# Kernel tuning notes

Hardware: AMD Instinct MI355X
Metric: run time of the kernel (lower is better)

Reference implementation:

```python
import jax, jax.numpy as jnp
import numpy as np

EPS = 1e-12  # clamp for sqrt stability in Gram-matrix distance

def _pairwise_euclid(X, Y):
    # [B,D],[M,D] -> [B,M] Euclidean distances via Gram trick (avoids [B,M,D] diff tensor)
    x2 = jnp.sum(X * X, axis=-1, keepdims=True)        # [B,1]
    y2 = jnp.sum(Y * Y, axis=-1)[None, :]              # [1,M]
    sq = x2 + y2 - 2.0 * (X @ Y.T)
    return jnp.sqrt(jnp.maximum(sq, EPS))

def setup_inputs() -> dict:
    key = jax.random.key(0)
    k1, k2, k3 = jax.random.split(key, 3)
    B, D = 4096, 128
    return {
        "rep_anchor": jax.random.normal(k1, (B, D), dtype=jnp.float32),
        "rep_pos": jax.random.normal(k2, (B, D), dtype=jnp.float32),
        "rep_neg": jax.random.normal(k3, (B, D), dtype=jnp.float32),
    }

def reference(rep_anchor, rep_pos, rep_neg):
    B = rep_anchor.shape[0]
    # distance_pos[i] = ||a_i - p_i||_2 (elementwise rows, like F.pairwise_distance)
    diff = rep_anchor - rep_pos
    distance_pos = jnp.sqrt(jnp.maximum(jnp.sum(diff * diff, axis=-1), EPS))  # [B]

    big = jnp.asarray(jnp.finfo(rep_anchor.dtype).max, rep_anchor.dtype)
    eye = jnp.eye(B, dtype=bool)
    # anchor-as-negative: exclude self (index i)
    d_aa = jnp.where(eye, big, _pairwise_euclid(rep_anchor, rep_anchor))  # [B,B]
    # pos-as-negative: rep_pos[i] is excluded for anchor i
    d_ap = jnp.where(eye, big, _pairwise_euclid(rep_anchor, rep_pos))    # [B,B]
    # all of rep_neg are negatives
    d_an = _pairwise_euclid(rep_anchor, rep_neg)                          # [B,B]

    hardest_neg = jnp.minimum(jnp.minimum(d_aa.min(axis=1), d_ap.min(axis=1)), d_an.min(axis=1))  # [B]
    # log1p(exp(x)) == softplus, computed stably
    loss_in_batch = jnp.logaddexp(0.0, distance_pos - hardest_neg)
    return jnp.mean(loss_in_batch)
```

## Files before the change

### kernel.cpp

```cpp
#include <hip/hip_runtime.h>
#include <math.h>

#define BDIM 4096
#define DDIM 128
#define EPSF 1e-12f
#define TI 128
#define TJc 128
#define NSPLIT 16
#define NSLICE (NSPLIT * 2)
#define ITILES (BDIM / TI)
#define JT 6
#define FLT_BIG 3.402823466e+38f
#define MATSZ (BDIM * DDIM)
#define YBUF (TJc * DDIM)

typedef __attribute__((ext_vector_type(8))) _Float16 f16x8;
typedef __attribute__((ext_vector_type(16))) float f32x16;

__device__ __forceinline__ void gload_lds16(const void* g, void* l) {
    __builtin_amdgcn_global_load_lds(
        (const __attribute__((address_space(1))) unsigned int*)(uintptr_t)g,
        (__attribute__((address_space(3))) unsigned int*)(unsigned int)(uintptr_t)l,
        16, 0, 0);
}

__device__ __forceinline__ unsigned int pack2h(float x, float y) {
    _Float16 hx = (_Float16)x, hy = (_Float16)y;
    unsigned short ux, uy;
    __builtin_memcpy(&ux, &hx, 2);
    __builtin_memcpy(&uy, &hy, 2);
    return (unsigned int)ux | ((unsigned int)uy << 16);
}

__global__ __launch_bounds__(256) void prep_kernel(
    const float* __restrict__ A, const float* __restrict__ P,
    const float* __restrict__ N, ushort* __restrict__ Xf,
    float* __restrict__ a2, float* __restrict__ p2,
    float* __restrict__ n2, float* __restrict__ dpos) {
    int row = (blockIdx.x * blockDim.x + threadIdx.x) >> 6;
    int lane = threadIdx.x & 63;
    if (row >= BDIM) return;
    const float2 av = *(const float2*)&A[row * DDIM + lane * 2];
    const float2 pv = *(const float2*)&P[row * DDIM + lane * 2];
    const float2 nv = *(const float2*)&N[row * DDIM + lane * 2];
    *(unsigned int*)&Xf[0 * MATSZ + row * DDIM + lane * 2] = pack2h(av.x, av.y);
    *(unsigned int*)&Xf[1 * MATSZ + row * DDIM + lane * 2] = pack2h(pv.x, pv.y);
    *(unsigned int*)&Xf[2 * MATSZ + row * DDIM + lane * 2] = pack2h(nv.x, nv.y);
    float sa = av.x * av.x + av.y * av.y;
    float sp = pv.x * pv.x + pv.y * pv.y;
    float sn = nv.x * nv.x + nv.y * nv.y;
    float dx = av.x - pv.x, dy = av.y - pv.y;
    float sd = dx * dx + dy * dy;
    #pragma unroll
    for (int off = 32; off; off >>= 1) {
        sa += __shfl_down(sa, off);
        sp += __shfl_down(sp, off);
        sn += __shfl_down(sn, off);
        sd += __shfl_down(sd, off);
    }
    if (lane == 0) {
        a2[row] = sa;
        p2[row] = sp;
        n2[row] = sn;
        dpos[row] = sqrtf(fmaxf(sd, EPSF));
    }
}

__global__ __launch_bounds__(256, 2) void minsq_kernel(
    const ushort* __restrict__ Xf,
    const float* __restrict__ a2, const float* __restrict__ p2,
    const float* __restrict__ n2, float* __restrict__ partial) {
    __shared__ __align__(16) ushort Y[2][YBUF];

    const int tid = threadIdx.x;
    const int w = tid >> 6;
    const int lane = tid & 63;
    const int rg = w >> 1;
    const int ch = w & 1;
    const int iTile = blockIdx.x;
    const int split = blockIdx.y;
    const int i0 = iTile * TI;
    const int jt0 = split * JT;
    const int sub = lane >> 4, s = lane & 15;

    {
        int m = jt0 >> 5, tc = jt0 & 31;
        const ushort* g = Xf + (size_t)m * MATSZ + (size_t)tc * TJc * DDIM;
        #pragma unroll
        for (int q = 0; q < 8; ++q) {
            int r = w * 32 + q * 4 + sub;
            int sp = s ^ (r & 15);
            gload_lds16(g + (size_t)r * DDIM + sp * 8,
                        &Y[0][(w * 32 + q * 4) * DDIM]);
        }
    }
    f16x8 a0[8], a1[8];
    {
        const ushort* r0 = Xf + (size_t)(i0 + rg * 64 + (lane & 31)) * DDIM;
        const ushort* r1 = r0 + 32 * DDIM;
        #pragma unroll
        for (int t = 0; t < 8; ++t) {
            int sl = t * 2 + (lane >> 5);
            a0[t] = *(const f16x8*)(r0 + sl * 8);
            a1[t] = *(const f16x8*)(r1 + sl * 8);
        }
    }
    float y2h0[JT], y2h1[JT];
    #pragma unroll
    for (int t = 0; t < JT; ++t) {
        int jt = jt0 + t, m = jt >> 5, tc = jt & 31;
        const float* y2g = (m == 0) ? a2 : ((m == 1) ? p2 : n2);
        int jb = tc * TJc + ch * 64 + (lane & 31);
        y2h0[t] = 0.5f * y2g[jb];
        y2h1[t] = 0.5f * y2g[jb + 32];
    }

    float minv0[16], minv1[16];
    #pragma unroll
    for (int g = 0; g < 16; ++g) { minv0[g] = FLT_BIG; minv1[g] = FLT_BIG; }

    #pragma unroll
    for (int idx = 0; idx < JT; ++idx) {
        if (idx + 1 < JT) {
            int jn = jt0 + idx + 1, m = jn >> 5, tc = jn & 31;
            const ushort* g = Xf + (size_t)m * MATSZ + (size_t)tc * TJc * DDIM;
            #pragma unroll
            for (int q = 0; q < 8; ++q) {
                int r = w * 32 + q * 4 + sub;
                int sp = s ^ (r & 15);
                gload_lds16(g + (size_t)r * DDIM + sp * 8,
                            &Y[(idx + 1) & 1][(w * 32 + q * 4) * DDIM]);
            }
            asm volatile("s_waitcnt vmcnt(8)" ::: "memory");
        } else {
            asm volatile("s_waitcnt vmcnt(0)" ::: "memory");
        }
        __builtin_amdgcn_sched_barrier(0);
        __builtin_amdgcn_s_barrier();
        __builtin_amdgcn_sched_barrier(0);

        const ushort* buf = &Y[idx & 1][0];
        const int rB0 = ch * 64 + (lane & 31);
        const int rB1 = rB0 + 32;
        f32x16 acc00 = {}, acc01 = {}, acc10 = {}, acc11 = {};
        __builtin_amdgcn_s_setprio(1);
        #pragma unroll
        for (int t = 0; t < 8; ++t) {
            int sl = t * 2 + (lane >> 5);
            f16x8 b0 = *(const f16x8*)&buf[rB0 * DDIM + (sl ^ (rB0 & 15)) * 8];
            f16x8 b1 = *(const f16x8*)&buf[rB1 * DDIM + (sl ^ (rB1 & 15)) * 8];
            acc00 = __builtin_amdgcn_mfma_f32_32x32x16_f16(a0[t], b0, acc00, 0, 0, 0);
            acc10 = __builtin_amdgcn_mfma_f32_32x32x16_f16(a1[t], b0, acc10, 0, 0, 0);
            acc01 = __builtin_amdgcn_mfma_f32_32x32x16_f16(a0[t], b1, acc01, 0, 0, 0);
            acc11 = __builtin_amdgcn_mfma_f32_32x32x16_f16(a1[t], b1, acc11, 0, 0, 0);
        }
        __builtin_amdgcn_s_setprio(0);

        {
            int jt = jt0 + idx, m = jt >> 5, tc = jt & 31;
            float yh0 = y2h0[idx], yh1 = y2h1[idx];
            if (m < 2 && tc == iTile) {
                int jg0 = tc * TJc + ch * 64 + (lane & 31);
                int jg1 = jg0 + 32;
                #pragma unroll
                for (int g = 0; g < 16; ++g) {
                    int rloc = (g & 3) + 8 * (g >> 2) + 4 * (lane >> 5);
                    int ig0 = i0 + rg * 64 + rloc;
                    int ig1 = ig0 + 32;
                    float c;
                    c = yh0 - acc00[g]; if (ig0 == jg0) c = FLT_BIG;
                    minv0[g] = fminf(minv0[g], c);
                    c = yh1 - acc01[g]; if (ig0 == jg1) c = FLT_BIG;
                    minv0[g] = fminf(minv0[g], c);
                    c = yh0 - acc10[g]; if (ig1 == jg0) c = FLT_BIG;
                    minv1[g] = fminf(minv1[g], c);
                    c = yh1 - acc11[g]; if (ig1 == jg1) c = FLT_BIG;
                    minv1[g] = fminf(minv1[g], c);
                }
            } else {
                #pragma unroll
                for (int g = 0; g < 16; ++g) {
                    minv0[g] = fminf(minv0[g], fminf(yh0 - acc00[g], yh1 - acc01[g]));
                    minv1[g] = fminf(minv1[g], fminf(yh0 - acc10[g], yh1 - acc11[g]));
                }
            }
        }
        __builtin_amdgcn_s_barrier();
    }

    #pragma unroll
    for (int off = 1; off < 32; off <<= 1) {
        #pragma unroll
        for (int g = 0; g < 16; ++g) {
            minv0[g] = fminf(minv0[g], __shfl_xor(minv0[g], off));
            minv1[g] = fminf(minv1[g], __shfl_xor(minv1[g], off));
        }
    }
    if ((lane & 31) == 0) {
        int hi = lane >> 5;
        int slice = split * 2 + ch;
        #pragma unroll
        for (int g = 0; g < 16; ++g) {
            int rloc = (g & 3) + 8 * (g >> 2) + 4 * hi;
            int ig = i0 + rg * 64 + rloc;
            partial[(size_t)ig * NSLICE + slice] = minv0[g];
            partial[(size_t)(ig + 32) * NSLICE + slice] = minv1[g];
        }
    }
}

__global__ __launch_bounds__(256) void lossA_kernel(
    const float* __restrict__ partial, const float* __restrict__ a2,
    const float* __restrict__ dpos, float* __restrict__ bsum) {
    __shared__ float red[4];
    int i = blockIdx.x * 256 + threadIdx.x;
    const float4* pr = (const float4*)&partial[(size_t)i * NSLICE];
    float mv = FLT_BIG;
    #pragma unroll
    for (int q = 0; q < NSLICE / 4; ++q) {
        float4 v = pr[q];
        mv = fminf(mv, fminf(fminf(v.x, v.y), fminf(v.z, v.w)));
    }
    float h2 = a2[i] + 2.0f * mv;
    float hardest = sqrtf(fmaxf(h2, EPSF));
    float x = dpos[i] - hardest;
    float sum = fmaxf(x, 0.f) + log1pf(expf(-fabsf(x)));
    #pragma unroll
    for (int off = 32; off; off >>= 1) sum += __shfl_down(sum, off);
    if ((threadIdx.x & 63) == 0) red[threadIdx.x >> 6] = sum;
    __syncthreads();
    if (threadIdx.x == 0)
        bsum[blockIdx.x] = red[0] + red[1] + red[2] + red[3];
}

__global__ void lossB_kernel(const float* __restrict__ bsum,
                             float* __restrict__ out) {
    float v = (threadIdx.x < 16) ? bsum[threadIdx.x] : 0.f;
    #pragma unroll
    for (int off = 32; off; off >>= 1) v += __shfl_down(v, off);
    if (threadIdx.x == 0) out[0] = v * (1.0f / BDIM);
}

extern "C" void kernel_launch(void* const* d_in, const int* in_sizes, int n_in,
                              void* d_out, int out_size, void* d_ws, size_t ws_size,
                              hipStream_t stream) {
    const float* A = (const float*)d_in[0];
    const float* P = (const float*)d_in[1];
    const float* N = (const float*)d_in[2];

    float* ws = (float*)d_ws;
    float* a2 = ws;
    float* p2 = ws + BDIM;
    float* n2 = ws + 2 * BDIM;
    float* dpos = ws + 3 * BDIM;
    float* bsum = ws + 4 * BDIM;
    float* partial = ws + 4 * BDIM + 64;
    ushort* Xf = (ushort*)(partial + (size_t)BDIM * NSLICE);

    prep_kernel<<<BDIM / 4, 256, 0, stream>>>(A, P, N, Xf, a2, p2, n2, dpos);
    dim3 grid2(ITILES, NSPLIT);
    minsq_kernel<<<grid2, 256, 0, stream>>>(Xf, a2, p2, n2, partial);
    lossA_kernel<<<16, 256, 0, stream>>>(partial, a2, dpos, bsum);
    lossB_kernel<<<1, 64, 0, stream>>>(bsum, (float*)d_out);
}
```

Measured before the change: 38.37 us.

## Load B tiles directly from global into registers, drop LDS staging and barriers

Removes the double-buffered LDS staging of the Y tiles (global_load_lds plus block barriers) and instead has each wave load its B fragments straight from global memory into registers, in two halves of four k-steps. The aim is to drop LDS traffic and block-wide synchronisation, and the smaller LDS footprint may allow more resident blocks. In exchange, each B row is now fetched redundantly by the two row-group waves through L1/L2, and the async prefetch overlap of the next tile is lost.

```diff
diff --git a/kernel.cpp b/kernel.cpp
--- a/kernel.cpp
+++ b/kernel.cpp
@@ -12,17 +12,9 @@
 #define JT 6
 #define FLT_BIG 3.402823466e+38f
 #define MATSZ (BDIM * DDIM)
-#define YBUF (TJc * DDIM)
 
 typedef __attribute__((ext_vector_type(8))) _Float16 f16x8;
 typedef __attribute__((ext_vector_type(16))) float f32x16;
-
-__device__ __forceinline__ void gload_lds16(const void* g, void* l) {
-    __builtin_amdgcn_global_load_lds(
-        (const __attribute__((address_space(1))) unsigned int*)(uintptr_t)g,
-        (__attribute__((address_space(3))) unsigned int*)(unsigned int)(uintptr_t)l,
-        16, 0, 0);
-}
 
 __device__ __forceinline__ unsigned int pack2h(float x, float y) {
     _Float16 hx = (_Float16)x, hy = (_Float16)y;
@@ -70,8 +62,6 @@
     const ushort* __restrict__ Xf,
     const float* __restrict__ a2, const float* __restrict__ p2,
     const float* __restrict__ n2, float* __restrict__ partial) {
-    __shared__ __align__(16) ushort Y[2][YBUF];
-
     const int tid = threadIdx.x;
     const int w = tid >> 6;
     const int lane = tid & 63;
@@ -81,28 +71,16 @@
     const int split = blockIdx.y;
     const int i0 = iTile * TI;
     const int jt0 = split * JT;
-    const int sub = lane >> 4, s = lane & 15;
-
-    {
-        int m = jt0 >> 5, tc = jt0 & 31;
-        const ushort* g = Xf + (size_t)m * MATSZ + (size_t)tc * TJc * DDIM;
-        #pragma unroll
-        for (int q = 0; q < 8; ++q) {
-            int r = w * 32 + q * 4 + sub;
-            int sp = s ^ (r & 15);
-            gload_lds16(g + (size_t)r * DDIM + sp * 8,
-                        &Y[0][(w * 32 + q * 4) * DDIM]);
-        }
-    }
+
     f16x8 a0[8], a1[8];
     {
-        const ushort* r0 = Xf + (size_t)(i0 + rg * 64 + (lane & 31)) * DDIM;
+        const ushort* r0 =
+            Xf + (size_t)(i0 + rg * 64 + (lane & 31)) * DDIM + (lane >> 5) * 8;
         const ushort* r1 = r0 + 32 * DDIM;
         #pragma unroll
         for (int t = 0; t < 8; ++t) {
-            int sl = t * 2 + (lane >> 5);
-            a0[t] = *(const f16x8*)(r0 + sl * 8);
-            a1[t] = *(const f16x8*)(r1 + sl * 8);
+            a0[t] = *(const f16x8*)(r0 + t * 16);
+            a1[t] = *(const f16x8*)(r1 + t * 16);
         }
     }
     float y2h0[JT], y2h1[JT];
@@ -121,43 +99,37 @@
 
     #pragma unroll
     for (int idx = 0; idx < JT; ++idx) {
-        if (idx + 1 < JT) {
-            int jn = jt0 + idx + 1, m = jn >> 5, tc = jn & 31;
-            const ushort* g = Xf + (size_t)m * MATSZ + (size_t)tc * TJc * DDIM;
+        const int jt = jt0 + idx;
+        const int m = jt >> 5;
+        const int tc = jt & 31;
+        const ushort* pb0 = Xf + (size_t)m * MATSZ +
+                            (size_t)(tc * TJc + ch * 64 + (lane & 31)) * DDIM +
+                            (lane >> 5) * 8;
+        const ushort* pb1 = pb0 + 32 * DDIM;
+
+        f32x16 acc00 = {}, acc01 = {}, acc10 = {}, acc11 = {};
+        #pragma unroll
+        for (int half = 0; half < 2; ++half) {
+            f16x8 b0[4], b1[4];
             #pragma unroll
-            for (int q = 0; q < 8; ++q) {
-                int r = w * 32 + q * 4 + sub;
-                int sp = s ^ (r & 15);
-                gload_lds16(g + (size_t)r * DDIM + sp * 8,
-                            &Y[(idx + 1) & 1][(w * 32 + q * 4) * DDIM]);
+            for (int q = 0; q < 4; ++q) {
+                int t = half * 4 + q;
+                b0[q] = *(const f16x8*)(pb0 + t * 16);
+                b1[q] = *(const f16x8*)(pb1 + t * 16);
             }
-            asm volatile("s_waitcnt vmcnt(8)" ::: "memory");
-        } else {
-            asm volatile("s_waitcnt vmcnt(0)" ::: "memory");
-        }
-        __builtin_amdgcn_sched_barrier(0);
-        __builtin_amdgcn_s_barrier();
-        __builtin_amdgcn_sched_barrier(0);
-
-        const ushort* buf = &Y[idx & 1][0];
-        const int rB0 = ch * 64 + (lane & 31);
-        const int rB1 = rB0 + 32;
-        f32x16 acc00 = {}, acc01 = {}, acc10 = {}, acc11 = {};
-        __builtin_amdgcn_s_setprio(1);
-        #pragma unroll
-        for (int t = 0; t < 8; ++t) {
-            int sl = t * 2 + (lane >> 5);
-            f16x8 b0 = *(const f16x8*)&buf[rB0 * DDIM + (sl ^ (rB0 & 15)) * 8];
-            f16x8 b1 = *(const f16x8*)&buf[rB1 * DDIM + (sl ^ (rB1 & 15)) * 8];
-            acc00 = __builtin_amdgcn_mfma_f32_32x32x16_f16(a0[t], b0, acc00, 0, 0, 0);
-            acc10 = __builtin_amdgcn_mfma_f32_32x32x16_f16(a1[t], b0, acc10, 0, 0, 0);
-            acc01 = __builtin_amdgcn_mfma_f32_32x32x16_f16(a0[t], b1, acc01, 0, 0, 0);
-            acc11 = __builtin_amdgcn_mfma_f32_32x32x16_f16(a1[t], b1, acc11, 0, 0, 0);
-        }
-        __builtin_amdgcn_s_setprio(0);
+            __builtin_amdgcn_s_setprio(1);
+            #pragma unroll
+            for (int q = 0; q < 4; ++q) {
+                int t = half * 4 + q;
+                acc00 = __builtin_amdgcn_mfma_f32_32x32x16_f16(a0[t], b0[q], acc00, 0, 0, 0);
+                acc10 = __builtin_amdgcn_mfma_f32_32x32x16_f16(a1[t], b0[q], acc10, 0, 0, 0);
+                acc01 = __builtin_amdgcn_mfma_f32_32x32x16_f16(a0[t], b1[q], acc01, 0, 0, 0);
+                acc11 = __builtin_amdgcn_mfma_f32_32x32x16_f16(a1[t], b1[q], acc11, 0, 0, 0);
+            }
+            __builtin_amdgcn_s_setprio(0);
+        }
 
         {
-            int jt = jt0 + idx, m = jt >> 5, tc = jt & 31;
             float yh0 = y2h0[idx], yh1 = y2h1[idx];
             if (m < 2 && tc == iTile) {
                 int jg0 = tc * TJc + ch * 64 + (lane & 31);
@@ -185,7 +157,6 @@
                 }
             }
         }
-        __builtin_amdgcn_s_barrier();
     }
 
     #pragma unroll
```

Result: slower. 45.76 us (+19.3%).
